# Performance work log

Measured on AMD Instinct MI355X. Metric: run time of the kernel, lower is better.

The kernel has to match this reference:

```python
import jax, jax.numpy as jnp
import numpy as np

V, E, H = 348, 512, 1024  # vocab, embed dim, GRU hidden


def gru_cell(x, h, w_ih, w_hh, b_ih, b_hh):
    # PyTorch GRUCell: gates ordered [r, z, n] along the 3H axis
    gi = x @ w_ih.T + b_ih            # [B, 3H]
    gh = h @ w_hh.T + b_hh            # [B, 3H]
    i_r, i_z, i_n = jnp.split(gi, 3, axis=-1)
    h_r, h_z, h_n = jnp.split(gh, 3, axis=-1)
    r = jax.nn.sigmoid(i_r + h_r)
    z = jax.nn.sigmoid(i_z + h_z)
    n = jnp.tanh(i_n + r * h_n)
    return (1.0 - z) * n + z * h


def setup_inputs() -> dict:
    key = jax.random.key(0)
    ks = jax.random.split(key, 20)
    B, T = 256, 128
    p = lambda k, shape: jax.random.normal(k, shape, dtype=jnp.float32) * 0.02
    return {
        "target": jax.random.randint(ks[0], (B, T), 0, V, dtype=jnp.int32),
        "bos": 1,
        "emb": p(ks[1], (V, E)),
        "w_ih1": p(ks[2], (3 * H, E)),  "w_hh1": p(ks[3], (3 * H, H)),
        "b_ih1": p(ks[4], (3 * H,)),    "b_hh1": p(ks[5], (3 * H,)),
        "w_ih2": p(ks[6], (3 * H, H)),  "w_hh2": p(ks[7], (3 * H, H)),
        "b_ih2": p(ks[8], (3 * H,)),    "b_hh2": p(ks[9], (3 * H,)),
        "w_ih3": p(ks[10], (3 * H, H)), "w_hh3": p(ks[11], (3 * H, H)),
        "b_ih3": p(ks[12], (3 * H,)),   "b_hh3": p(ks[13], (3 * H,)),
        "w_out": p(ks[14], (V, H)),     "b_out": p(ks[15], (V,)),
    }


def reference(target, bos, emb, w_ih1, w_hh1, b_ih1, b_hh1,
              w_ih2, w_hh2, b_ih2, b_hh2,
              w_ih3, w_hh3, b_ih3, b_hh3, w_out, b_out):
    B, T = target.shape
    # input tokens = [<bos>, target[:, :-1]]
    x_in = jnp.concatenate(
        [jnp.full((B, 1), bos, dtype=target.dtype), target[:, :-1]], axis=1)
    h0 = jnp.zeros((B, H), jnp.float32)
    lp0 = jnp.zeros((B,), jnp.float32)

    def step(carry, xt):
        h1, h2, h3, lp = carry
        tok, tgt = xt                     # [B], [B]
        e = emb[tok]                      # [B, E]
        h1 = gru_cell(e, h1, w_ih1, w_hh1, b_ih1, b_hh1)
        h2 = gru_cell(h1, h2, w_ih2, w_hh2, b_ih2, b_hh2)
        h3 = gru_cell(h2, h3, w_ih3, w_hh3, b_ih3, b_hh3)
        logits = h3 @ w_out.T + b_out     # [B, V]
        logp = jax.nn.log_softmax(logits, axis=-1)
        # NLLLoss in source = sum(one_hot(tgt) * log_prob) = gathered log-prob
        lp = lp + jnp.take_along_axis(logp, tgt[:, None], axis=1)[:, 0]
        return (h1, h2, h3, lp), None

    (_, _, _, log_probs), _ = jax.lax.scan(
        step, (h0, h0, h0, lp0), (x_in.T, target.T))
    return log_probs
```

## Files before the change

### kernel.cpp

```cpp
#include <hip/hip_runtime.h>
#include <hip/hip_bf16.h>
#include <cstdint>

constexpr int kT = 128;
constexpr int kB = 256;
constexpr int kE = 512;
constexpr int kH = 1024;
constexpr int kV = 348;
constexpr int kNG = 3072;
constexpr int NB = 208;

constexpr float kScale = 32.f;
constexpr float kInvSS = 1.f / 1024.f;

typedef float f4v __attribute__((ext_vector_type(4)));
typedef unsigned short u16;
typedef unsigned char u8;

__device__ __forceinline__ u8 f2e4m3(float x) {
  int p = __builtin_amdgcn_cvt_pk_fp8_f32(x, x, 0, false);
  return (u8)(p & 0xff);
}

__device__ __forceinline__ uint64_t ldv_u64(const void* p) {
  return __hip_atomic_load((const uint64_t*)p, __ATOMIC_RELAXED, __HIP_MEMORY_SCOPE_AGENT);
}
__device__ __forceinline__ void stv_u8(u8* p, u8 v) {
  __hip_atomic_store(p, v, __ATOMIC_RELAXED, __HIP_MEMORY_SCOPE_AGENT);
}

__device__ __forceinline__ int permn(int n) {
  int gate = n >> 10, j = n & 1023;
  return ((j >> 4) * 48) + gate * 16 + (j & 15);
}

struct Params {
  const int* target; const int* bosp; const float* b_out;
  const u8 *w1i, *w1h, *w2i, *w2h, *w3i, *w3h, *wout, *embb;
  const float *bi1, *bh1, *bi2, *bh2, *bi3, *bh3;
  float *h1f, *h2f, *h3f;
  u8    *h1b, *h2b, *h3b;
  float *lp;
  unsigned *acnt; unsigned *gflag;
};

union SMem {
  struct { u8 A[128 * 128]; u8 B[96 * 128]; } mm;
  float logits[16 * 400];
};

__device__ __forceinline__ void gbar(unsigned* acnt, unsigned* gflag, unsigned s) {
  asm volatile("s_waitcnt vmcnt(0)" ::: "memory");
  __syncthreads();
  if (threadIdx.x == 0) {
    const unsigned g = blockIdx.x & 31u;
    __hip_atomic_fetch_add(&acnt[g * 16], 1u, __ATOMIC_RELAXED, __HIP_MEMORY_SCOPE_AGENT);
    if (blockIdx.x == 0) {
      for (;;) {
        unsigned sum = 0;
#pragma unroll
        for (int i = 0; i < 32; ++i)
          sum += __hip_atomic_load(&acnt[i * 16], __ATOMIC_RELAXED, __HIP_MEMORY_SCOPE_AGENT);
        if (sum >= (unsigned)NB * (s + 1u)) break;
        __builtin_amdgcn_s_sleep(4);
      }
#pragma unroll
      for (int i = 0; i < 32; ++i)
        __hip_atomic_store(&gflag[i * 16], s + 1u, __ATOMIC_RELAXED, __HIP_MEMORY_SCOPE_AGENT);
    } else {
      while (__hip_atomic_load(&gflag[g * 16], __ATOMIC_RELAXED, __HIP_MEMORY_SCOPE_AGENT) <= s)
        __builtin_amdgcn_s_sleep(8);
    }
    asm volatile("" ::: "memory");
  }
  __syncthreads();
}

#define LOAD_A(dst, k0)                                                      \
  _Pragma("unroll")                                                          \
  for (int p = 0; p < 4; ++p) {                                              \
    int id = p * 256 + t, r = id >> 3, c = id & 7;                           \
    if (EMB) {                                                               \
      int tok = (u == 0) ? bos : target[(b0 + r) * kT + (u - 1)];            \
      uint4 v = *(const uint4*)&Asrc[(size_t)tok * K + (k0) + c * 16];       \
      dst[p][0] = ((uint64_t)v.y << 32) | v.x;                               \
      dst[p][1] = ((uint64_t)v.w << 32) | v.z;                               \
    } else {                                                                 \
      const u8* srcp = Asrc + (size_t)(b0 + r) * kH + (k0) + c * 16;         \
      dst[p][0] = ldv_u64(srcp); dst[p][1] = ldv_u64(srcp + 8);              \
    }                                                                        \
  }

#define LOAD_B(k0)                                                           \
  _Pragma("unroll")                                                          \
  for (int p = 0; p < 3; ++p) {                                              \
    int id = p * 256 + t, r = id >> 3, c = id & 7;                           \
    rb[p] = *(const uint4*)&W[(size_t)(n0 + r) * K + (k0) + c * 16];         \
  }

#define WR_AB(srcA)                                                          \
  _Pragma("unroll")                                                          \
  for (int p = 0; p < 4; ++p) {                                              \
    int id = p * 256 + t, r = id >> 3, c = id & 7;                           \
    const int u0 = c * 2, rx = r & 15;                                       \
    u8* base = &sm.mm.A[r * 128];                                            \
    *(uint64_t*)(base + 8 * (u0 ^ rx)) = srcA[p][0];                         \
    *(uint64_t*)(base + 8 * ((u0 + 1) ^ rx)) = srcA[p][1];                   \
  }                                                                          \
  _Pragma("unroll")                                                          \
  for (int p = 0; p < 3; ++p) {                                              \
    int id = p * 256 + t, r = id >> 3, c = id & 7;                           \
    const int u0 = c * 2, rx = r & 15;                                       \
    u8* base = &sm.mm.B[r * 128];                                            \
    *(uint64_t*)(base + 8 * (u0 ^ rx)) = (uint64_t)rb[p].x | ((uint64_t)rb[p].y << 32); \
    *(uint64_t*)(base + 8 * ((u0 + 1) ^ rx)) = (uint64_t)rb[p].z | ((uint64_t)rb[p].w << 32); \
  }

#define MFMA_TILE()                                                          \
  _Pragma("unroll")                                                          \
  for (int kk = 0; kk < 128; kk += 32) {                                     \
    const int swz = 8 * (((kk >> 3) + q) ^ li);                              \
    long a[4], bb[3];                                                        \
    _Pragma("unroll")                                                        \
    for (int m2 = 0; m2 < 4; ++m2)                                           \
      a[m2] = *(const long*)&sm.mm.A[(64 * wm + 16 * m2 + li) * 128 + swz];  \
    _Pragma("unroll")                                                        \
    for (int g = 0; g < 3; ++g)                                              \
      bb[g] = *(const long*)&sm.mm.B[(48 * wg + 16 * g + li) * 128 + swz];   \
    _Pragma("unroll")                                                        \
    for (int m2 = 0; m2 < 4; ++m2) {                                         \
      aR[m2] = __builtin_amdgcn_mfma_f32_16x16x32_fp8_fp8(a[m2], bb[0], aR[m2], 0, 0, 0); \
      aZ[m2] = __builtin_amdgcn_mfma_f32_16x16x32_fp8_fp8(a[m2], bb[1], aZ[m2], 0, 0, 0); \
      aN[m2] = __builtin_amdgcn_mfma_f32_16x16x32_fp8_fp8(a[m2], bb[2], aN[m2], 0, 0, 0); \
    }                                                                        \
  }

template<int K, bool EMB>
__device__ __forceinline__ void mm_phase(SMem& sm, const u8* __restrict__ Asrc,
    const u8* __restrict__ W, int b0, int n0,
    f4v* aR, f4v* aZ, f4v* aN,
    const int* __restrict__ target, int bos, int u)
{
  const int t = threadIdx.x, lane = t & 63, wv = t >> 6;
  const int wm = wv >> 1, wg = wv & 1, li = lane & 15, q = lane >> 4;
  constexpr int NT = K / 128;
  uint64_t raE[4][2], raO[4][2];
  uint4 rb[3];

  LOAD_A(raE, 0)
  LOAD_A(raO, 128)
  LOAD_B(0)

#pragma unroll 1
  for (int it = 0; it < NT; it += 2) {
    __syncthreads();
    WR_AB(raE)
    __syncthreads();
    if (it + 2 < NT) { LOAD_A(raE, (it + 2) * 128) }
    LOAD_B((it + 1) * 128)
    MFMA_TILE()
    __syncthreads();
    WR_AB(raO)
    __syncthreads();
    if (it + 3 < NT) { LOAD_A(raO, (it + 3) * 128) }
    if (it + 2 < NT) { LOAD_B((it + 2) * 128) }
    MFMA_TILE()
  }
}

template<int K1, bool L1>
__device__ void do_L(SMem& sm, const u8* __restrict__ xsrc,
                     const u8* __restrict__ hbPrev, const float* __restrict__ hfPrev,
                     const u8* __restrict__ Wih, const u8* __restrict__ Whh,
                     const float* __restrict__ biP, const float* __restrict__ bhP,
                     float* __restrict__ hfOut, u8* __restrict__ hbOut,
                     const int* __restrict__ target, int bos, int u, int mt, int jt)
{
  const int b0 = mt * 128, j0 = jt * 32, n0 = jt * 96;
  f4v aR[4], aZ[4], aNi[4], aNh[4];
#pragma unroll
  for (int i = 0; i < 4; ++i) {
    aR[i] = f4v{0.f,0.f,0.f,0.f}; aZ[i] = f4v{0.f,0.f,0.f,0.f};
    aNi[i] = f4v{0.f,0.f,0.f,0.f}; aNh[i] = f4v{0.f,0.f,0.f,0.f};
  }
  mm_phase<K1, L1>(sm, xsrc, Wih, b0, n0, aR, aZ, aNi, target, bos, u);
  mm_phase<kH, false>(sm, hbPrev, Whh, b0, n0, aR, aZ, aNh, target, bos, u);

  const int t = threadIdx.x, lane = t & 63, wv = t >> 6;
  const int wm = wv >> 1, wg = wv & 1, li = lane & 15, q = lane >> 4;
  const int j = j0 + 16 * wg + li;
  const int cr = n0 + 48 * wg + li;
  const float bR = biP[cr] + bhP[cr];
  const float bZ = biP[cr + 16] + bhP[cr + 16];
  const float biN = biP[cr + 32], bhN = bhP[cr + 32];
  float hold[4][4];
#pragma unroll
  for (int m2 = 0; m2 < 4; ++m2)
#pragma unroll
    for (int r = 0; r < 4; ++r) {
      int b = b0 + 64 * wm + 16 * m2 + 4 * q + r;
      hold[m2][r] = hfPrev[(size_t)b * kH + j];
    }
#pragma unroll
  for (int m2 = 0; m2 < 4; ++m2)
#pragma unroll
    for (int r = 0; r < 4; ++r) {
      int b = b0 + 64 * wm + 16 * m2 + 4 * q + r;
      float rg = 1.f / (1.f + __expf(-(aR[m2][r] * kInvSS + bR)));
      float zg = 1.f / (1.f + __expf(-(aZ[m2][r] * kInvSS + bZ)));
      float np = (aNi[m2][r] * kInvSS + biN) + rg * (aNh[m2][r] * kInvSS + bhN);
      float nh = 2.f / (1.f + __expf(-2.f * np)) - 1.f;
      float hnew = (1.f - zg) * nh + zg * hold[m2][r];
      hfOut[(size_t)b * kH + j] = hnew;
      stv_u8(&hbOut[(size_t)b * kH + j], f2e4m3(hnew * kScale));
    }
}

__device__ void do_E(SMem& sm, const u8* __restrict__ h3b, const u8* __restrict__ wo,
                     const float* __restrict__ b_out, const int* __restrict__ target,
                     float* __restrict__ lp, int u, int tile)
{
  const int b0 = tile * 16;
  const int t = threadIdx.x, lane = t & 63, wv = t >> 6;
  const int li = lane & 15, q = lane >> 4;
  f4v acc[6];
#pragma unroll
  for (int f = 0; f < 6; ++f) acc[f] = f4v{0.f, 0.f, 0.f, 0.f};

  const u8* ap = h3b + (size_t)(b0 + li) * kH + q * 8;
  uint64_t aCur = ldv_u64(ap);
  uint64_t bCur[6], bNx[6];
#pragma unroll
  for (int f = 0; f < 6; ++f)
    bCur[f] = *(const uint64_t*)&wo[(size_t)(96 * wv + 16 * f + li) * kH + q * 8];
  for (int k0 = 0; k0 < kH; k0 += 32) {
    uint64_t aNx = 0;
    if (k0 + 32 < kH) {
      aNx = ldv_u64(ap + k0 + 32);
#pragma unroll
      for (int f = 0; f < 6; ++f)
        bNx[f] = *(const uint64_t*)&wo[(size_t)(96 * wv + 16 * f + li) * kH + k0 + 32 + q * 8];
    }
#pragma unroll
    for (int f = 0; f < 6; ++f)
      acc[f] = __builtin_amdgcn_mfma_f32_16x16x32_fp8_fp8((long)aCur, (long)bCur[f], acc[f], 0, 0, 0);
    aCur = aNx;
#pragma unroll
    for (int f = 0; f < 6; ++f) bCur[f] = bNx[f];
  }
#pragma unroll
  for (int f = 0; f < 6; ++f) {
    int n = 96 * wv + 16 * f + li;
    if (n < kV) {
      float bo = b_out[n];
#pragma unroll
      for (int r = 0; r < 4; ++r)
        sm.logits[(4 * q + r) * 400 + n] = acc[f][r] * kInvSS + bo;
    }
  }
  __syncthreads();
  int m = 4 * wv + q;
  int b = b0 + m;
  float mx = -1e30f;
  for (int cc = li; cc < kV; cc += 16) mx = fmaxf(mx, sm.logits[m * 400 + cc]);
#pragma unroll
  for (int d = 1; d < 16; d <<= 1) mx = fmaxf(mx, __shfl_xor(mx, d, 16));
  float se = 0.f;
  for (int cc = li; cc < kV; cc += 16) se += __expf(sm.logits[m * 400 + cc] - mx);
#pragma unroll
  for (int d = 1; d < 16; d <<= 1) se += __shfl_xor(se, d, 16);
  int tgt = target[b * kT + u];
  float logp = sm.logits[m * 400 + tgt] - mx - __logf(se);
  if (li == 0) lp[b] += logp;
}

__global__ __launch_bounds__(256, 1) void rnn_main(Params P)
{
  __shared__ SMem sm;
  const int bid = blockIdx.x;
  const int bos = P.bosp[0];
  const size_t HS = (size_t)kB * kH;

  const int local = bid & 63;
  const int mt = (local >> 3) & 1;
  const int jt = (local & 7) | ((local >> 4) << 3);

  for (int s = 0; s < kT + 3; ++s) {
    if (bid < 64) {
      int u = s;
      if (u < kT)
        do_L<kE, true>(sm, P.embb,
                       P.h1b + (size_t)((u - 1) & 1) * HS, P.h1f + (size_t)((u - 1) & 1) * HS,
                       P.w1i, P.w1h, P.bi1, P.bh1,
                       P.h1f + (size_t)(u & 1) * HS, P.h1b + (size_t)(u & 1) * HS,
                       P.target, bos, u, mt, jt);
    } else if (bid < 128) {
      int u = s - 1;
      if (u >= 0 && u < kT)
        do_L<kH, false>(sm, P.h1b + (size_t)(u & 1) * HS,
                        P.h2b + (size_t)((u - 1) & 1) * HS, P.h2f + (size_t)((u - 1) & 1) * HS,
                        P.w2i, P.w2h, P.bi2, P.bh2,
                        P.h2f + (size_t)(u & 1) * HS, P.h2b + (size_t)(u & 1) * HS,
                        P.target, bos, u, mt, jt);
    } else if (bid < 192) {
      int u = s - 2;
      if (u >= 0 && u < kT)
        do_L<kH, false>(sm, P.h2b + (size_t)(u & 1) * HS,
                        P.h3b + (size_t)((u - 1) & 1) * HS, P.h3f + (size_t)((u - 1) & 1) * HS,
                        P.w3i, P.w3h, P.bi3, P.bh3,
                        P.h3f + (size_t)(u & 1) * HS, P.h3b + (size_t)(u & 1) * HS,
                        P.target, bos, u, mt, jt);
    } else {
      int u = s - 3;
      if (u >= 0 && u < kT)
        do_E(sm, P.h3b + (size_t)(u & 1) * HS, P.wout, P.b_out, P.target, P.lp, u, bid - 192);
    }
    gbar(P.acnt, P.gflag, (unsigned)s);
  }
}

__global__ void k_conv_w(const float* __restrict__ w, u8* __restrict__ wp, int K, int logK) {
  int idx = blockIdx.x * 256 + threadIdx.x;
  if (idx >= kNG * K) return;
  int n = idx >> logK, k = idx & (K - 1);
  wp[(size_t)permn(n) * K + k] = f2e4m3(w[idx] * kScale);
}
__global__ void k_conv_b(const float* __restrict__ b, float* __restrict__ bp) {
  int idx = blockIdx.x * 256 + threadIdx.x;
  if (idx < kNG) bp[permn(idx)] = b[idx];
}
__global__ void k_conv_wout(const float* __restrict__ w, u8* __restrict__ wp) {
  int idx = blockIdx.x * 256 + threadIdx.x;
  if (idx >= 384 * kH) return;
  int n = idx >> 10, k = idx & 1023;
  wp[idx] = (n < kV) ? f2e4m3(w[(size_t)n * kH + k] * kScale) : (u8)0;
}
__global__ void k_conv_emb(const float* __restrict__ e, u8* __restrict__ ep) {
  int idx = blockIdx.x * 256 + threadIdx.x;
  if (idx < kV * kE) ep[idx] = f2e4m3(e[idx] * kScale);
}

extern "C" void kernel_launch(void* const* d_in, const int* in_sizes, int n_in,
                              void* d_out, int out_size, void* d_ws, size_t ws_size,
                              hipStream_t stream)
{
  const int*   target = (const int*)d_in[0];
  const int*   bosp   = (const int*)d_in[1];
  const float* emb    = (const float*)d_in[2];
  const float* w_ih1  = (const float*)d_in[3];
  const float* w_hh1  = (const float*)d_in[4];
  const float* b_ih1  = (const float*)d_in[5];
  const float* b_hh1  = (const float*)d_in[6];
  const float* w_ih2  = (const float*)d_in[7];
  const float* w_hh2  = (const float*)d_in[8];
  const float* b_ih2  = (const float*)d_in[9];
  const float* b_hh2  = (const float*)d_in[10];
  const float* w_ih3  = (const float*)d_in[11];
  const float* w_hh3  = (const float*)d_in[12];
  const float* b_ih3  = (const float*)d_in[13];
  const float* b_hh3  = (const float*)d_in[14];
  const float* w_out  = (const float*)d_in[15];
  const float* b_out  = (const float*)d_in[16];

  char* ws = (char*)d_ws;
  size_t off = 0;
  auto alloc = [&](size_t bytes) -> void* {
    void* p = ws + off;
    off = (off + bytes + 511) & ~(size_t)511;
    return p;
  };
  u8* w1i = (u8*)alloc((size_t)kNG * kE);
  u8* w1h = (u8*)alloc((size_t)kNG * kH);
  u8* w2i = (u8*)alloc((size_t)kNG * kH);
  u8* w2h = (u8*)alloc((size_t)kNG * kH);
  u8* w3i = (u8*)alloc((size_t)kNG * kH);
  u8* w3h = (u8*)alloc((size_t)kNG * kH);
  u8* wo  = (u8*)alloc((size_t)384 * kH);
  u8* eb  = (u8*)alloc((size_t)kV * kE);
  float* bi1 = (float*)alloc(kNG * 4);
  float* bh1 = (float*)alloc(kNG * 4);
  float* bi2 = (float*)alloc(kNG * 4);
  float* bh2 = (float*)alloc(kNG * 4);
  float* bi3 = (float*)alloc(kNG * 4);
  float* bh3 = (float*)alloc(kNG * 4);
  float* h1f = (float*)alloc((size_t)2 * kB * kH * 4);
  float* h2f = (float*)alloc((size_t)2 * kB * kH * 4);
  float* h3f = (float*)alloc((size_t)2 * kB * kH * 4);
  u8* h1b = (u8*)alloc((size_t)2 * kB * kH);
  u8* h2b = (u8*)alloc((size_t)2 * kB * kH);
  u8* h3b = (u8*)alloc((size_t)2 * kB * kH);
  unsigned* bar = (unsigned*)alloc(4096);
  (void)ws_size; (void)in_sizes; (void)n_in; (void)out_size;

  k_conv_w<<<(kNG * kE + 255) / 256, 256, 0, stream>>>(w_ih1, w1i, kE, 9);
  k_conv_w<<<(kNG * kH + 255) / 256, 256, 0, stream>>>(w_hh1, w1h, kH, 10);
  k_conv_w<<<(kNG * kH + 255) / 256, 256, 0, stream>>>(w_ih2, w2i, kH, 10);
  k_conv_w<<<(kNG * kH + 255) / 256, 256, 0, stream>>>(w_hh2, w2h, kH, 10);
  k_conv_w<<<(kNG * kH + 255) / 256, 256, 0, stream>>>(w_ih3, w3i, kH, 10);
  k_conv_w<<<(kNG * kH + 255) / 256, 256, 0, stream>>>(w_hh3, w3h, kH, 10);
  k_conv_b<<<(kNG + 255) / 256, 256, 0, stream>>>(b_ih1, bi1);
  k_conv_b<<<(kNG + 255) / 256, 256, 0, stream>>>(b_hh1, bh1);
  k_conv_b<<<(kNG + 255) / 256, 256, 0, stream>>>(b_ih2, bi2);
  k_conv_b<<<(kNG + 255) / 256, 256, 0, stream>>>(b_hh2, bh2);
  k_conv_b<<<(kNG + 255) / 256, 256, 0, stream>>>(b_ih3, bi3);
  k_conv_b<<<(kNG + 255) / 256, 256, 0, stream>>>(b_hh3, bh3);
  k_conv_wout<<<(384 * kH + 255) / 256, 256, 0, stream>>>(w_out, wo);
  k_conv_emb<<<(kV * kE + 255) / 256, 256, 0, stream>>>(emb, eb);

  hipMemsetAsync(h1f, 0, (size_t)3 * 2 * kB * kH * 4, stream);
  hipMemsetAsync(h1b, 0, (size_t)3 * 2 * kB * kH, stream);
  hipMemsetAsync(bar, 0, 4096, stream);
  hipMemsetAsync(d_out, 0, (size_t)kB * 4, stream);

  Params P;
  P.target = target; P.bosp = bosp; P.b_out = b_out;
  P.w1i = w1i; P.w1h = w1h; P.w2i = w2i; P.w2h = w2h; P.w3i = w3i; P.w3h = w3h;
  P.wout = wo; P.embb = eb;
  P.bi1 = bi1; P.bh1 = bh1; P.bi2 = bi2; P.bh2 = bh2; P.bi3 = bi3; P.bh3 = bh3;
  P.h1f = h1f; P.h2f = h2f; P.h3f = h3f;
  P.h1b = h1b; P.h2b = h2b; P.h3b = h3b;
  P.lp = (float*)d_out;
  P.acnt = bar; P.gflag = bar + 512;

  rnn_main<<<dim3(NB), dim3(256), 0, stream>>>(P);
}
```

Baseline: 4.000 ms.

## Double-buffer weight tile registers and use LDS-only barriers in GEMM loop

Gives the B (weight) tile its own even/odd register buffers, so weight loads are issued two tiles ahead like the A loads, giving global latency more time to hide. It also replaces __syncthreads with a barrier that waits only on LDS counters, so outstanding global loads are not drained at each barrier. The cost is more VGPRs for the extra B buffer. The LDS-only barrier relies on global-load data being waited on where it is consumed.

```diff
diff --git a/kernel.cpp b/kernel.cpp
--- a/kernel.cpp
+++ b/kernel.cpp
@@ -48,6 +48,8 @@
   struct { u8 A[128 * 128]; u8 B[96 * 128]; } mm;
   float logits[16 * 400];
 };
+
+#define BAR_LDS() asm volatile("s_waitcnt lgkmcnt(0)\n\ts_barrier" ::: "memory")
 
 __device__ __forceinline__ void gbar(unsigned* acnt, unsigned* gflag, unsigned s) {
   asm volatile("s_waitcnt vmcnt(0)" ::: "memory");
@@ -91,14 +93,14 @@
     }                                                                        \
   }
 
-#define LOAD_B(k0)                                                           \
+#define LOAD_B(dst, k0)                                                      \
   _Pragma("unroll")                                                          \
   for (int p = 0; p < 3; ++p) {                                              \
     int id = p * 256 + t, r = id >> 3, c = id & 7;                           \
-    rb[p] = *(const uint4*)&W[(size_t)(n0 + r) * K + (k0) + c * 16];         \
-  }
-
-#define WR_AB(srcA)                                                          \
+    dst[p] = *(const uint4*)&W[(size_t)(n0 + r) * K + (k0) + c * 16];        \
+  }
+
+#define WR_AB(srcA, srcB)                                                    \
   _Pragma("unroll")                                                          \
   for (int p = 0; p < 4; ++p) {                                              \
     int id = p * 256 + t, r = id >> 3, c = id & 7;                           \
@@ -112,8 +114,8 @@
     int id = p * 256 + t, r = id >> 3, c = id & 7;                           \
     const int u0 = c * 2, rx = r & 15;                                       \
     u8* base = &sm.mm.B[r * 128];                                            \
-    *(uint64_t*)(base + 8 * (u0 ^ rx)) = (uint64_t)rb[p].x | ((uint64_t)rb[p].y << 32); \
-    *(uint64_t*)(base + 8 * ((u0 + 1) ^ rx)) = (uint64_t)rb[p].z | ((uint64_t)rb[p].w << 32); \
+    *(uint64_t*)(base + 8 * (u0 ^ rx)) = (uint64_t)srcB[p].x | ((uint64_t)srcB[p].y << 32); \
+    *(uint64_t*)(base + 8 * ((u0 + 1) ^ rx)) = (uint64_t)srcB[p].z | ((uint64_t)srcB[p].w << 32); \
   }
 
 #define MFMA_TILE()                                                          \
@@ -145,25 +147,24 @@
   const int wm = wv >> 1, wg = wv & 1, li = lane & 15, q = lane >> 4;
   constexpr int NT = K / 128;
   uint64_t raE[4][2], raO[4][2];
-  uint4 rb[3];
+  uint4 rbE[3], rbO[3];
 
   LOAD_A(raE, 0)
+  LOAD_B(rbE, 0)
   LOAD_A(raO, 128)
-  LOAD_B(0)
+  LOAD_B(rbO, 128)
 
 #pragma unroll 1
   for (int it = 0; it < NT; it += 2) {
-    __syncthreads();
-    WR_AB(raE)
-    __syncthreads();
-    if (it + 2 < NT) { LOAD_A(raE, (it + 2) * 128) }
-    LOAD_B((it + 1) * 128)
+    BAR_LDS();
+    WR_AB(raE, rbE)
+    BAR_LDS();
+    if (it + 2 < NT) { LOAD_A(raE, (it + 2) * 128) LOAD_B(rbE, (it + 2) * 128) }
     MFMA_TILE()
-    __syncthreads();
-    WR_AB(raO)
-    __syncthreads();
-    if (it + 3 < NT) { LOAD_A(raO, (it + 3) * 128) }
-    if (it + 2 < NT) { LOAD_B((it + 2) * 128) }
+    BAR_LDS();
+    WR_AB(raO, rbO)
+    BAR_LDS();
+    if (it + 3 < NT) { LOAD_A(raO, (it + 3) * 128) LOAD_B(rbO, (it + 3) * 128) }
     MFMA_TILE()
   }
 }
```

Measured after the change: 4.033 ms. Within noise of the previous version (+0.8%).
